# Optimization experiments

Hardware: AMD Instinct MI355X
Metric: run time of the kernel (lower is better)

The kernel has to match this reference:

```python
import jax, jax.numpy as jnp
import numpy as np

N_NODES = 50000
N_EDGES = 800000
IN_DIM = 128
OUT_DIM = 128
NUM_RELS = 8


def setup_inputs() -> dict:
    key = jax.random.key(0)
    k_feat, k_rel, k_w, k_src, k_dst, k_rt = jax.random.split(key, 6)
    feat = jax.random.normal(k_feat, (N_NODES, IN_DIM), dtype=jnp.float32)
    # xavier_uniform over (in_dim, out_dim) fan
    limit = float(np.sqrt(6.0 / (IN_DIM + OUT_DIM)))
    rel_emb = jax.random.uniform(k_rel, (NUM_RELS, IN_DIM, OUT_DIM), dtype=jnp.float32,
                                 minval=-limit, maxval=limit)
    edge_weight = jax.random.uniform(k_w, (N_EDGES,), dtype=jnp.float32)
    src = jax.random.randint(k_src, (N_EDGES,), 0, N_NODES, dtype=jnp.int32)
    dst = jax.random.randint(k_dst, (N_EDGES,), 0, N_NODES, dtype=jnp.int32)
    rel_type = jax.random.randint(k_rt, (N_EDGES,), 0, NUM_RELS, dtype=jnp.int32)
    return {"feat": feat, "rel_emb": rel_emb, "edge_weight": edge_weight,
            "src": src, "dst": dst, "rel_type": rel_type}


def reference(feat, rel_emb, edge_weight, src, dst, rel_type):
    # src_feat: [E, in] gather of source-node features
    src_feat = feat[src]
    num_rels = rel_emb.shape[0]
    # Equivalent to bmm(src_feat[:,None,:], rel_emb[rel_type]).squeeze(1)
    # but avoids materializing the [E, in, out] per-edge weight tensor:
    # loop over the small fixed relation set with masked accumulation.
    msg = jnp.zeros((src_feat.shape[0], rel_emb.shape[2]), dtype=src_feat.dtype)
    for r in range(num_rels):
        mask = (rel_type == r)[:, None]
        msg = msg + jnp.where(mask, src_feat @ rel_emb[r], jnp.zeros((), dtype=src_feat.dtype))
    msg = msg * edge_weight[:, None]
    # copy_e + sum aggregation onto destination nodes: [N, out]
    return jax.ops.segment_sum(msg, dst, num_segments=feat.shape[0])
```

## Files before the change

kernel.cpp:

```cpp
#include <hip/hip_runtime.h>
#include <stdint.h>

#define N_NODES   50000
#define N_EDGES   800000
#define IN_DIM    128
#define OUT_DIM   128
#define NUM_RELS  8
#define THREADS   256

typedef _Float16 half_t;
typedef _Float16 half2v __attribute__((ext_vector_type(2)));
typedef _Float16 half4v __attribute__((ext_vector_type(4)));
typedef _Float16 half8 __attribute__((ext_vector_type(8)));
typedef float floatx4 __attribute__((ext_vector_type(4)));


#define NBINS3    N_NODES
#define NB3       ((NBINS3 + 1023) / 1024)

#define WS_Y2     0
#define WS_OFF    102400000
#define WS_WT     102600064
#define WS_BASE   102862208
#define WS_WGT    106062208
#define WS_HIST   107662208
#define WS_BSUM   107862208
#define WS_NEED   (size_t)107862464

#define HIST_BLOCKS ((N_EDGES + 511) / 512)
__global__ void prep_hist_kernel(const float* __restrict__ rel_emb, half_t* __restrict__ WT,
                                 const int* __restrict__ dst, int* __restrict__ hist) {
    int b = blockIdx.x;
    if (b < 512) {
        int t = b * 256 + threadIdx.x;
        int r = t >> 14, k = (t >> 7) & 127, n = t & 127;
        WT[(size_t)((r << 7) | n) * 128 + k] = (half_t)rel_emb[t];
    } else {
        int i = (b - 512) * 512 + threadIdx.x;
        int d0 = (i < N_EDGES) ? dst[i] : -1;
        int d1 = (i + 256 < N_EDGES) ? dst[i + 256] : -1;
        if (d0 >= 0) atomicAdd(&hist[d0], 1);
        if (d1 >= 0) atomicAdd(&hist[d1], 1);
    }
}

__global__ void scan1_kernel(const int* __restrict__ hist, int* __restrict__ bsum) {
    __shared__ int sh[256];
    int b = blockIdx.x, t = threadIdx.x;
    int i0 = b * 1024 + t * 4;
    int s = 0;
    #pragma unroll
    for (int j = 0; j < 4; j++) { int idx = i0 + j; if (idx < NBINS3) s += hist[idx]; }
    sh[t] = s; __syncthreads();
    for (int o = 128; o > 0; o >>= 1) { if (t < o) sh[t] += sh[t + o]; __syncthreads(); }
    if (t == 0) bsum[b] = sh[0];
}

__global__ void scan2_kernel(int* __restrict__ bsum, int* __restrict__ off) {
    __shared__ int sh[64];
    int t = threadIdx.x;
    int v = (t < NB3) ? bsum[t] : 0;
    sh[t] = v; __syncthreads();
    for (int o = 1; o < 64; o <<= 1) {
        int x = (t >= o) ? sh[t - o] : 0;
        __syncthreads();
        sh[t] += x;
        __syncthreads();
    }
    if (t < NB3) bsum[t] = sh[t] - v;
    if (t == 0) off[NBINS3] = N_EDGES;
}

__global__ void scan3_kernel(const int* __restrict__ hist, const int* __restrict__ boff,
                             int* __restrict__ off, int* __restrict__ cursors) {
    __shared__ int sh[256];
    int b = blockIdx.x, t = threadIdx.x;
    int i0 = b * 1024 + t * 4;
    int v[4]; int s = 0;
    #pragma unroll
    for (int j = 0; j < 4; j++) { int idx = i0 + j; v[j] = (idx < NBINS3) ? hist[idx] : 0; s += v[j]; }
    sh[t] = s; __syncthreads();
    for (int o = 1; o < 256; o <<= 1) {
        int x = (t >= o) ? sh[t - o] : 0;
        __syncthreads();
        sh[t] += x;
        __syncthreads();
    }
    int run = sh[t] - s + boff[b];
    #pragma unroll
    for (int j = 0; j < 4; j++) {
        int idx = i0 + j;
        if (idx < NBINS3) { off[idx] = run; cursors[idx] = run; }
        run += v[j];
    }
}

template<bool GUARD>
__device__ __forceinline__ void gemm_body(const float* __restrict__ feat,
                                          half_t* __restrict__ Ws,
                                          half_t* __restrict__ y2,
                                          int m0, int n0, int wave, int lane) {
    const int q = lane >> 4, l16 = lane & 15;
    const int wm0 = m0 + wave * 32;

    float4 fr[2][4][2];
    #pragma unroll
    for (int ms = 0; ms < 2; ms++) {
        int node = wm0 + ms * 16 + l16;
        const float* fb = feat + (size_t)node * 128 + q * 8;
        bool ok = !GUARD || node < N_NODES;
        #pragma unroll
        for (int kk = 0; kk < 4; kk++)
            #pragma unroll
            for (int h = 0; h < 2; h++) {
                float4 v = {0.f, 0.f, 0.f, 0.f};
                if (ok) v = *(const float4*)(fb + kk * 32 + h * 4);
                fr[ms][kk][h] = v;
            }
    }
    __syncthreads();

    half8 bf[2][4];
    #pragma unroll
    for (int ms = 0; ms < 2; ms++)
        #pragma unroll
        for (int kk = 0; kk < 4; kk++) {
            half8 hb;
            hb[0] = (half_t)fr[ms][kk][0].x; hb[1] = (half_t)fr[ms][kk][0].y;
            hb[2] = (half_t)fr[ms][kk][0].z; hb[3] = (half_t)fr[ms][kk][0].w;
            hb[4] = (half_t)fr[ms][kk][1].x; hb[5] = (half_t)fr[ms][kk][1].y;
            hb[6] = (half_t)fr[ms][kk][1].z; hb[7] = (half_t)fr[ms][kk][1].w;
            bf[ms][kk] = hb;
        }

    floatx4 acc[8][2];
    #pragma unroll
    for (int nt = 0; nt < 8; nt++)
        #pragma unroll
        for (int ms = 0; ms < 2; ms++) acc[nt][ms] = (floatx4){0.f, 0.f, 0.f, 0.f};

    #pragma unroll
    for (int kk = 0; kk < 4; kk++) {
        #pragma unroll
        for (int nt = 0; nt < 8; nt++) {
            int row = nt * 16 + l16;
            int phys = (kk * 4 + q) ^ (l16 & 7);
            half8 a = *(const half8*)(Ws + row * 128 + phys * 8);
            acc[nt][0] = __builtin_amdgcn_mfma_f32_16x16x32_f16(a, bf[0][kk], acc[nt][0], 0, 0, 0);
            acc[nt][1] = __builtin_amdgcn_mfma_f32_16x16x32_f16(a, bf[1][kk], acc[nt][1], 0, 0, 0);
        }
    }

    __syncthreads();
    #pragma unroll
    for (int nt = 0; nt < 8; nt++)
        #pragma unroll
        for (int ms = 0; ms < 2; ms++) {
            int nl = wave * 32 + ms * 16 + l16;
            int c  = nt * 4 + q;
            int p  = (c + nl) & 31;
            half4v hv;
            hv[0] = (half_t)acc[nt][ms][0]; hv[1] = (half_t)acc[nt][ms][1];
            hv[2] = (half_t)acc[nt][ms][2]; hv[3] = (half_t)acc[nt][ms][3];
            *(half4v*)(Ws + nl * 128 + p * 4) = hv;
        }
    #pragma unroll
    for (int i = 0; i < 8; i++) {
        int nl  = wave * 32 + i * 4 + (lane >> 4);
        int c16 = lane & 15;
        int p0 = (2 * c16 + nl) & 31;
        int p1 = (2 * c16 + 1 + nl) & 31;
        uint2 lo = *(const uint2*)(Ws + nl * 128 + p0 * 4);
        uint2 hi = *(const uint2*)(Ws + nl * 128 + p1 * 4);
        int node = m0 + nl;
        if (!GUARD || node < N_NODES) {
            uint4 v; v.x = lo.x; v.y = lo.y; v.z = hi.x; v.w = hi.y;
            *(uint4*)(y2 + (size_t)node * 1024 + n0 + c16 * 8) = v;
        }
    }
}

#define FUSE_BLOCKS 6256
__global__ __launch_bounds__(THREADS) void fused_kernel(
    const float* __restrict__ feat, const half_t* __restrict__ WT,
    half_t* __restrict__ y2,
    const int* __restrict__ dst, const int* __restrict__ src,
    const int* __restrict__ rel, const float* __restrict__ ew,
    int* __restrict__ cursors, int* __restrict__ base, half_t* __restrict__ wgt) {
    __shared__ half_t Ws[128 * 128];
    const int bid = blockIdx.x;
    const int t = threadIdx.x;

    if (((bid >> 3) & 1) == 0) {
        int work = (bid & 7) * 391 + (bid >> 4);
        int mt = work >> 3, nt8 = work & 7;
        const int m0 = mt * 128, n0 = nt8 * 128;
        const int wave = t >> 6, lane = t & 63;

        for (int i = t; i < 2048; i += THREADS) {
            int row = i >> 4, lc = i & 15;
            int phys = lc ^ (row & 7);
            *(uint4*)&Ws[row * 128 + phys * 8] =
                *(const uint4*)(WT + (size_t)(n0 + row) * 128 + lc * 8);
        }
        if (m0 + 128 <= N_NODES)
            gemm_body<false>(feat, Ws, y2, m0, n0, wave, lane);
        else
            gemm_body<true>(feat, Ws, y2, m0, n0, wave, lane);
    } else {
        int sblock = (bid >> 4) * 8 + (bid & 7);
        if (sblock >= 3125) return;
        int i = sblock * 256 + t;
        int pos = atomicAdd(&cursors[dst[i]], 1);
        base[pos] = src[i] * 1024 + rel[i] * 128;
        wgt[pos] = (half_t)ew[i];
    }
}

__global__ __launch_bounds__(THREADS) void gather_kernel(
    const half_t* __restrict__ y2, const int* __restrict__ base,
    const half_t* __restrict__ wgt, const int* __restrict__ off,
    float* __restrict__ out) {
    int g = blockIdx.x * 4 + (threadIdx.x >> 6);
    int lane = threadIdx.x & 63;
    int beg = off[g], end = off[g + 1];
    const half_t* yb = y2 + lane * 2;
    float ax = 0.f, ay = 0.f, cx = 0.f, cy = 0.f;
    int e = beg;
    for (; e + 8 <= end; e += 8) {
        int b0 = base[e], b1 = base[e + 1], b2 = base[e + 2], b3 = base[e + 3];
        int b4 = base[e + 4], b5 = base[e + 5], b6 = base[e + 6], b7 = base[e + 7];
        half2v v0 = *(const half2v*)(yb + b0);
        half2v v1 = *(const half2v*)(yb + b1);
        half2v v2 = *(const half2v*)(yb + b2);
        half2v v3 = *(const half2v*)(yb + b3);
        half2v v4 = *(const half2v*)(yb + b4);
        half2v v5 = *(const half2v*)(yb + b5);
        half2v v6 = *(const half2v*)(yb + b6);
        half2v v7 = *(const half2v*)(yb + b7);
        float w0 = (float)wgt[e],     w1 = (float)wgt[e + 1];
        float w2 = (float)wgt[e + 2], w3 = (float)wgt[e + 3];
        float w4 = (float)wgt[e + 4], w5 = (float)wgt[e + 5];
        float w6 = (float)wgt[e + 6], w7 = (float)wgt[e + 7];
        ax += w0 * (float)v0[0] + w1 * (float)v1[0];
        ay += w0 * (float)v0[1] + w1 * (float)v1[1];
        cx += w2 * (float)v2[0] + w3 * (float)v3[0];
        cy += w2 * (float)v2[1] + w3 * (float)v3[1];
        ax += w4 * (float)v4[0] + w5 * (float)v5[0];
        ay += w4 * (float)v4[1] + w5 * (float)v5[1];
        cx += w6 * (float)v6[0] + w7 * (float)v7[0];
        cy += w6 * (float)v6[1] + w7 * (float)v7[1];
    }
    for (; e + 2 <= end; e += 2) {
        int b0 = base[e], b1 = base[e + 1];
        float w0 = (float)wgt[e], w1 = (float)wgt[e + 1];
        half2v v0 = *(const half2v*)(yb + b0);
        half2v v1 = *(const half2v*)(yb + b1);
        ax += w0 * (float)v0[0] + w1 * (float)v1[0];
        ay += w0 * (float)v0[1] + w1 * (float)v1[1];
    }
    if (e < end) {
        int b0 = base[e];
        float w0 = (float)wgt[e];
        half2v v0 = *(const half2v*)(yb + b0);
        cx += w0 * (float)v0[0];
        cy += w0 * (float)v0[1];
    }
    float2 o; o.x = ax + cx; o.y = ay + cy;
    *(float2*)(out + (size_t)g * 128 + lane * 2) = o;
}

__global__ void naive_kernel(const float* __restrict__ feat, const float* __restrict__ rel_emb,
                             const float* __restrict__ ew, const int* __restrict__ src,
                             const int* __restrict__ dst, const int* __restrict__ rel,
                             float* __restrict__ out) {
    int wave = (blockIdx.x * blockDim.x + threadIdx.x) >> 6;
    int lane = threadIdx.x & 63;
    if (wave >= N_EDGES) return;
    const float* f = feat + (size_t)src[wave] * IN_DIM;
    const float* W = rel_emb + (size_t)rel[wave] * IN_DIM * OUT_DIM;
    float w = ew[wave];
    float a0 = 0.f, a1 = 0.f;
    for (int k = 0; k < IN_DIM; k++) {
        float fv = f[k];
        a0 += fv * W[k * OUT_DIM + lane];
        a1 += fv * W[k * OUT_DIM + 64 + lane];
    }
    int d = dst[wave];
    atomicAdd(&out[(size_t)d * OUT_DIM + lane], a0 * w);
    atomicAdd(&out[(size_t)d * OUT_DIM + 64 + lane], a1 * w);
}

extern "C" void kernel_launch(void* const* d_in, const int* in_sizes, int n_in,
                              void* d_out, int out_size, void* d_ws, size_t ws_size,
                              hipStream_t stream) {
    const float* feat    = (const float*)d_in[0];
    const float* rel_emb = (const float*)d_in[1];
    const float* ew      = (const float*)d_in[2];
    const int*   src     = (const int*)d_in[3];
    const int*   dst     = (const int*)d_in[4];
    const int*   rel     = (const int*)d_in[5];
    float* out = (float*)d_out;

    if (ws_size >= WS_NEED) {
        char* ws = (char*)d_ws;
        half_t* y2    = (half_t*)(ws + WS_Y2);
        int*    off   = (int*)(ws + WS_OFF);
        half_t* WT    = (half_t*)(ws + WS_WT);
        int*    basep = (int*)(ws + WS_BASE);
        half_t* wgt   = (half_t*)(ws + WS_WGT);
        int*    hist  = (int*)(ws + WS_HIST);
        int*    bsum  = (int*)(ws + WS_BSUM);

        hipMemsetAsync(hist, 0, (size_t)NBINS3 * 4, stream);
        prep_hist_kernel<<<512 + HIST_BLOCKS, THREADS, 0, stream>>>(rel_emb, WT, dst, hist);
        scan1_kernel<<<NB3, 256, 0, stream>>>(hist, bsum);
        scan2_kernel<<<1, 64, 0, stream>>>(bsum, off);
        scan3_kernel<<<NB3, 256, 0, stream>>>(hist, bsum, off, hist);
        fused_kernel<<<FUSE_BLOCKS, THREADS, 0, stream>>>(feat, WT, y2, dst, src, rel, ew,
                                                          hist, basep, wgt);
        gather_kernel<<<N_NODES / 4, THREADS, 0, stream>>>(y2, basep, wgt, off, out);
    } else {
        hipMemsetAsync(d_out, 0, (size_t)out_size * sizeof(float), stream);
        const long long total = (long long)N_EDGES * 64;
        const int blocks = (int)((total + THREADS - 1) / THREADS);
        naive_kernel<<<blocks, THREADS, 0, stream>>>(feat, rel_emb, ew, src, dst, rel, out);
    }
}
```

Measured before the change: 255.4 us.

## Fuse dst histogram into GEMM kernel, single-block scan, pack edge records

```diff
diff --git a/kernel.cpp b/kernel.cpp
--- a/kernel.cpp
+++ b/kernel.cpp
@@ -16,82 +16,55 @@
 
 
 #define NBINS3    N_NODES
-#define NB3       ((NBINS3 + 1023) / 1024)
 
 #define WS_Y2     0
-#define WS_OFF    102400000
-#define WS_WT     102600064
-#define WS_BASE   102862208
-#define WS_WGT    106062208
-#define WS_HIST   107662208
-#define WS_BSUM   107862208
-#define WS_NEED   (size_t)107862464
-
-#define HIST_BLOCKS ((N_EDGES + 511) / 512)
-__global__ void prep_hist_kernel(const float* __restrict__ rel_emb, half_t* __restrict__ WT,
-                                 const int* __restrict__ dst, int* __restrict__ hist) {
-    int b = blockIdx.x;
-    if (b < 512) {
-        int t = b * 256 + threadIdx.x;
-        int r = t >> 14, k = (t >> 7) & 127, n = t & 127;
-        WT[(size_t)((r << 7) | n) * 128 + k] = (half_t)rel_emb[t];
-    } else {
-        int i = (b - 512) * 512 + threadIdx.x;
-        int d0 = (i < N_EDGES) ? dst[i] : -1;
-        int d1 = (i + 256 < N_EDGES) ? dst[i + 256] : -1;
-        if (d0 >= 0) atomicAdd(&hist[d0], 1);
-        if (d1 >= 0) atomicAdd(&hist[d1], 1);
-    }
-}
-
-__global__ void scan1_kernel(const int* __restrict__ hist, int* __restrict__ bsum) {
-    __shared__ int sh[256];
-    int b = blockIdx.x, t = threadIdx.x;
-    int i0 = b * 1024 + t * 4;
-    int s = 0;
-    #pragma unroll
-    for (int j = 0; j < 4; j++) { int idx = i0 + j; if (idx < NBINS3) s += hist[idx]; }
-    sh[t] = s; __syncthreads();
-    for (int o = 128; o > 0; o >>= 1) { if (t < o) sh[t] += sh[t + o]; __syncthreads(); }
-    if (t == 0) bsum[b] = sh[0];
-}
-
-__global__ void scan2_kernel(int* __restrict__ bsum, int* __restrict__ off) {
-    __shared__ int sh[64];
-    int t = threadIdx.x;
-    int v = (t < NB3) ? bsum[t] : 0;
-    sh[t] = v; __syncthreads();
-    for (int o = 1; o < 64; o <<= 1) {
-        int x = (t >= o) ? sh[t - o] : 0;
+#define WS_WT     102400000
+#define WS_REC    102662144
+#define WS_HIST   105862144
+#define WS_NEED   (size_t)106062144
+
+__global__ void prep_wt_kernel(const float* __restrict__ rel_emb, half_t* __restrict__ WT) {
+    int t = blockIdx.x * blockDim.x + threadIdx.x;
+    int r = t >> 14, k = (t >> 7) & 127, n = t & 127;
+    WT[(size_t)((r << 7) | n) * 128 + k] = (half_t)rel_emb[t];
+}
+
+__global__ __launch_bounds__(1024) void scan_all_kernel(int* __restrict__ hist) {
+    __shared__ int sh[1024];
+    const int t = threadIdx.x;
+    int carry = 0;
+    for (int c = 0; c < 13; c++) {
+        int i0 = c * 4096 + t * 4;
+        int v0 = (i0     < NBINS3) ? hist[i0]     : 0;
+        int v1 = (i0 + 1 < NBINS3) ? hist[i0 + 1] : 0;
+        int v2 = (i0 + 2 < NBINS3) ? hist[i0 + 2] : 0;
+        int v3 = (i0 + 3 < NBINS3) ? hist[i0 + 3] : 0;
+        int s = v0 + v1 + v2 + v3;
+        sh[t] = s; __syncthreads();
+        for (int o = 1; o < 1024; o <<= 1) {
+            int x = (t >= o) ? sh[t - o] : 0;
+            __syncthreads();
+            sh[t] += x;
+            __syncthreads();
+        }
+        int run = carry + sh[t] - s;
+        if (i0     < NBINS3) hist[i0]     = run; run += v0;
+        if (i0 + 1 < NBINS3) hist[i0 + 1] = run; run += v1;
+        if (i0 + 2 < NBINS3) hist[i0 + 2] = run; run += v2;
+        if (i0 + 3 < NBINS3) hist[i0 + 3] = run;
+        carry += sh[1023];
         __syncthreads();
-        sh[t] += x;
-        __syncthreads();
-    }
-    if (t < NB3) bsum[t] = sh[t] - v;
-    if (t == 0) off[NBINS3] = N_EDGES;
-}
-
-__global__ void scan3_kernel(const int* __restrict__ hist, const int* __restrict__ boff,
-                             int* __restrict__ off, int* __restrict__ cursors) {
-    __shared__ int sh[256];
-    int b = blockIdx.x, t = threadIdx.x;
-    int i0 = b * 1024 + t * 4;
-    int v[4]; int s = 0;
-    #pragma unroll
-    for (int j = 0; j < 4; j++) { int idx = i0 + j; v[j] = (idx < NBINS3) ? hist[idx] : 0; s += v[j]; }
-    sh[t] = s; __syncthreads();
-    for (int o = 1; o < 256; o <<= 1) {
-        int x = (t >= o) ? sh[t - o] : 0;
-        __syncthreads();
-        sh[t] += x;
-        __syncthreads();
-    }
-    int run = sh[t] - s + boff[b];
-    #pragma unroll
-    for (int j = 0; j < 4; j++) {
-        int idx = i0 + j;
-        if (idx < NBINS3) { off[idx] = run; cursors[idx] = run; }
-        run += v[j];
+    }
+}
+
+__global__ void scatter_kernel(const int* __restrict__ dst, const int* __restrict__ src,
+                               const int* __restrict__ rel, const float* __restrict__ ew,
+                               int* __restrict__ cursors, unsigned* __restrict__ rec) {
+    int i = blockIdx.x * blockDim.x + threadIdx.x;
+    if (i < N_EDGES) {
+        int pos = atomicAdd(&cursors[dst[i]], 1);
+        unsigned w13 = (unsigned)(ew[i] * 8192.0f);
+        rec[pos] = (w13 << 19) | ((unsigned)rel[i] << 16) | (unsigned)src[i];
     }
 }
 
@@ -180,19 +153,19 @@
     }
 }
 
-#define FUSE_BLOCKS 6256
-__global__ __launch_bounds__(THREADS) void fused_kernel(
+#define FUSEA_BLOCKS (8 * 588)
+__global__ __launch_bounds__(THREADS) void fused_gh_kernel(
     const float* __restrict__ feat, const half_t* __restrict__ WT,
-    half_t* __restrict__ y2,
-    const int* __restrict__ dst, const int* __restrict__ src,
-    const int* __restrict__ rel, const float* __restrict__ ew,
-    int* __restrict__ cursors, int* __restrict__ base, half_t* __restrict__ wgt) {
+    half_t* __restrict__ y2, const int* __restrict__ dst, int* __restrict__ hist) {
     __shared__ half_t Ws[128 * 128];
     const int bid = blockIdx.x;
+    const int xcd = bid & 7, s = bid >> 3;
     const int t = threadIdx.x;
 
-    if (((bid >> 3) & 1) == 0) {
-        int work = (bid & 7) * 391 + (bid >> 4);
+    if (s % 3 != 2) {
+        int gidx = (s / 3) * 2 + (s % 3);
+        if (gidx >= 391) return;
+        int work = xcd * 391 + gidx;
         int mt = work >> 3, nt8 = work & 7;
         const int m0 = mt * 128, n0 = nt8 * 128;
         const int wave = t >> 6, lane = t & 63;
@@ -208,28 +181,36 @@
         else
             gemm_body<true>(feat, Ws, y2, m0, n0, wave, lane);
     } else {
-        int sblock = (bid >> 4) * 8 + (bid & 7);
-        if (sblock >= 3125) return;
-        int i = sblock * 256 + t;
-        int pos = atomicAdd(&cursors[dst[i]], 1);
-        base[pos] = src[i] * 1024 + rel[i] * 128;
-        wgt[pos] = (half_t)ew[i];
+        int hb = xcd * 196 + s / 3;
+        int i = hb * 512 + t;
+        int d0 = (i < N_EDGES) ? dst[i] : -1;
+        int d1 = (i + 256 < N_EDGES) ? dst[i + 256] : -1;
+        if (d0 >= 0) atomicAdd(&hist[d0], 1);
+        if (d1 >= 0) atomicAdd(&hist[d1], 1);
     }
 }
 
 __global__ __launch_bounds__(THREADS) void gather_kernel(
-    const half_t* __restrict__ y2, const int* __restrict__ base,
-    const half_t* __restrict__ wgt, const int* __restrict__ off,
-    float* __restrict__ out) {
+    const half_t* __restrict__ y2, const unsigned* __restrict__ rec,
+    const int* __restrict__ cur, float* __restrict__ out) {
     int g = blockIdx.x * 4 + (threadIdx.x >> 6);
     int lane = threadIdx.x & 63;
-    int beg = off[g], end = off[g + 1];
+    int beg = (g > 0) ? cur[g - 1] : 0;
+    int end = cur[g];
     const half_t* yb = y2 + lane * 2;
     float ax = 0.f, ay = 0.f, cx = 0.f, cy = 0.f;
     int e = beg;
     for (; e + 8 <= end; e += 8) {
-        int b0 = base[e], b1 = base[e + 1], b2 = base[e + 2], b3 = base[e + 3];
-        int b4 = base[e + 4], b5 = base[e + 5], b6 = base[e + 6], b7 = base[e + 7];
+        unsigned r0 = rec[e],     r1 = rec[e + 1], r2 = rec[e + 2], r3 = rec[e + 3];
+        unsigned r4 = rec[e + 4], r5 = rec[e + 5], r6 = rec[e + 6], r7 = rec[e + 7];
+        int b0 = (int)((r0 & 0xFFFFu) << 10) | (int)(((r0 >> 16) & 7u) << 7);
+        int b1 = (int)((r1 & 0xFFFFu) << 10) | (int)(((r1 >> 16) & 7u) << 7);
+        int b2 = (int)((r2 & 0xFFFFu) << 10) | (int)(((r2 >> 16) & 7u) << 7);
+        int b3 = (int)((r3 & 0xFFFFu) << 10) | (int)(((r3 >> 16) & 7u) << 7);
+        int b4 = (int)((r4 & 0xFFFFu) << 10) | (int)(((r4 >> 16) & 7u) << 7);
+        int b5 = (int)((r5 & 0xFFFFu) << 10) | (int)(((r5 >> 16) & 7u) << 7);
+        int b6 = (int)((r6 & 0xFFFFu) << 10) | (int)(((r6 >> 16) & 7u) << 7);
+        int b7 = (int)((r7 & 0xFFFFu) << 10) | (int)(((r7 >> 16) & 7u) << 7);
         half2v v0 = *(const half2v*)(yb + b0);
         half2v v1 = *(const half2v*)(yb + b1);
         half2v v2 = *(const half2v*)(yb + b2);
@@ -238,10 +219,11 @@
         half2v v5 = *(const half2v*)(yb + b5);
         half2v v6 = *(const half2v*)(yb + b6);
         half2v v7 = *(const half2v*)(yb + b7);
-        float w0 = (float)wgt[e],     w1 = (float)wgt[e + 1];
-        float w2 = (float)wgt[e + 2], w3 = (float)wgt[e + 3];
-        float w4 = (float)wgt[e + 4], w5 = (float)wgt[e + 5];
-        float w6 = (float)wgt[e + 6], w7 = (float)wgt[e + 7];
+        const float ws = 1.0f / 8192.0f;
+        float w0 = (float)(r0 >> 19) * ws, w1 = (float)(r1 >> 19) * ws;
+        float w2 = (float)(r2 >> 19) * ws, w3 = (float)(r3 >> 19) * ws;
+        float w4 = (float)(r4 >> 19) * ws, w5 = (float)(r5 >> 19) * ws;
+        float w6 = (float)(r6 >> 19) * ws, w7 = (float)(r7 >> 19) * ws;
         ax += w0 * (float)v0[0] + w1 * (float)v1[0];
         ay += w0 * (float)v0[1] + w1 * (float)v1[1];
         cx += w2 * (float)v2[0] + w3 * (float)v3[0];
@@ -251,20 +233,13 @@
         cx += w6 * (float)v6[0] + w7 * (float)v7[0];
         cy += w6 * (float)v6[1] + w7 * (float)v7[1];
     }
-    for (; e + 2 <= end; e += 2) {
-        int b0 = base[e], b1 = base[e + 1];
-        float w0 = (float)wgt[e], w1 = (float)wgt[e + 1];
-        half2v v0 = *(const half2v*)(yb + b0);
-        half2v v1 = *(const half2v*)(yb + b1);
-        ax += w0 * (float)v0[0] + w1 * (float)v1[0];
-        ay += w0 * (float)v0[1] + w1 * (float)v1[1];
-    }
-    if (e < end) {
-        int b0 = base[e];
-        float w0 = (float)wgt[e];
-        half2v v0 = *(const half2v*)(yb + b0);
-        cx += w0 * (float)v0[0];
-        cy += w0 * (float)v0[1];
+    for (; e < end; e++) {
+        unsigned r = rec[e];
+        int b = (int)((r & 0xFFFFu) << 10) | (int)(((r >> 16) & 7u) << 7);
+        float w = (float)(r >> 19) * (1.0f / 8192.0f);
+        half2v v = *(const half2v*)(yb + b);
+        ax += w * (float)v[0];
+        ay += w * (float)v[1];
     }
     float2 o; o.x = ax + cx; o.y = ay + cy;
     *(float2*)(out + (size_t)g * 128 + lane * 2) = o;
@@ -302,24 +277,21 @@
     const int*   rel     = (const int*)d_in[5];
     float* out = (float*)d_out;
 
+    const int eb = (N_EDGES + THREADS - 1) / THREADS;
+
     if (ws_size >= WS_NEED) {
         char* ws = (char*)d_ws;
-        half_t* y2    = (half_t*)(ws + WS_Y2);
-        int*    off   = (int*)(ws + WS_OFF);
-        half_t* WT    = (half_t*)(ws + WS_WT);
-        int*    basep = (int*)(ws + WS_BASE);
-        half_t* wgt   = (half_t*)(ws + WS_WGT);
-        int*    hist  = (int*)(ws + WS_HIST);
-        int*    bsum  = (int*)(ws + WS_BSUM);
+        half_t*   y2   = (half_t*)(ws + WS_Y2);
+        half_t*   WT   = (half_t*)(ws + WS_WT);
+        unsigned* rec  = (unsigned*)(ws + WS_REC);
+        int*      hist = (int*)(ws + WS_HIST);
 
         hipMemsetAsync(hist, 0, (size_t)NBINS3 * 4, stream);
-        prep_hist_kernel<<<512 + HIST_BLOCKS, THREADS, 0, stream>>>(rel_emb, WT, dst, hist);
-        scan1_kernel<<<NB3, 256, 0, stream>>>(hist, bsum);
-        scan2_kernel<<<1, 64, 0, stream>>>(bsum, off);
-        scan3_kernel<<<NB3, 256, 0, stream>>>(hist, bsum, off, hist);
-        fused_kernel<<<FUSE_BLOCKS, THREADS, 0, stream>>>(feat, WT, y2, dst, src, rel, ew,
-                                                          hist, basep, wgt);
-        gather_kernel<<<N_NODES / 4, THREADS, 0, stream>>>(y2, basep, wgt, off, out);
+        prep_wt_kernel<<<512, THREADS, 0, stream>>>(rel_emb, WT);
+        fused_gh_kernel<<<FUSEA_BLOCKS, THREADS, 0, stream>>>(feat, WT, y2, dst, hist);
+        scan_all_kernel<<<1, 1024, 0, stream>>>(hist);
+        scatter_kernel<<<eb, THREADS, 0, stream>>>(dst, src, rel, ew, hist, rec);
+        gather_kernel<<<N_NODES / 4, THREADS, 0, stream>>>(y2, rec, hist, out);
     } else {
         hipMemsetAsync(d_out, 0, (size_t)out_size * sizeof(float), stream);
         const long long total = (long long)N_EDGES * 64;
```

Result: slower. 265.4 us (+3.9%).
